# Optimization experiments

Measured on AMD Instinct MI355X. Metric: run time of the kernel, lower is better.

Reference implementation:

```python
import jax, jax.numpy as jnp
import numpy as np
from jax import lax


def _f(x, t, params):
    # Neural-ODE vector field: MLP acting on last dim (t unused, as allowed by arbitrary f)
    W1, b1, W2 = params
    return jnp.tanh(x @ W1 + b1) @ W2


def _euler_step(f, x, t, dt, params):
    return x + dt * f(x, t, params)


def _rk4_step(f, x, t, dt, params):
    # Replicates the source tableau EXACTLY, including its c-index offsets
    # (k2 uses t + c[0]*dt = t, k3 uses t + c[1]*dt, k4 uses t + c[2]*dt).
    c = (0.0, 0.5, 0.5, 1.0)
    k1 = f(x, t, params)
    k2 = f(x + dt * (0.5 * k1), t + c[0] * dt, params)
    k3 = f(x + dt * (0.5 * k2), t + c[1] * dt, params)
    k4 = f(x + dt * k3, t + c[2] * dt, params)
    return x + dt * (k1 / 6.0 + k2 / 3.0 + k3 / 3.0 + k4 / 6.0)


def _integrate(step, f, x, ts, params):
    # fixed_odeint with t = ts[k], dt = ts[k+1]-ts[k]; returns final state only
    dts = ts[1:] - ts[:-1]
    def body(xc, tdt):
        t, dt = tdt
        return step(f, xc, t, dt, params), None
    xf, _ = lax.scan(body, x, (ts[:-1], dts))
    return xf


def setup_inputs() -> dict:
    key = jax.random.key(0)
    k1, k2, k3 = jax.random.split(key, 3)
    n_sub, batch, d, h = 16, 256, 1024, 4096
    B = jax.random.normal(k1, (n_sub, batch, d), jnp.float32)
    t_span = jnp.arange(n_sub, dtype=jnp.float32)
    W1 = jax.random.normal(k2, (d, h), jnp.float32) * 0.02
    b1 = jnp.zeros((h,), jnp.float32)
    W2 = jax.random.normal(k3, (h, d), jnp.float32) * 0.02
    return {"B": B, "t_span": t_span, "W1": W1, "b1": b1, "W2": W2,
            "fine_steps": 8, "maxiter": 2}


def reference(B, t_span, W1, b1, W2, fine_steps, maxiter):
    params = (W1, b1, W2)
    n = B.shape[0]                       # n_subinterv
    dt = t_span[1] - t_span[0]
    sub_ts = jnp.linspace(0.0, dt, fine_steps)
    # Original: i = 0; while i <= maxiter: i += 1; body(i)  ->  i = 1..maxiter+1
    for i in range(1, maxiter + 2):
        # coarse (Euler) and fine (RK4) sweeps over all remaining nodes, vectorized
        B_coarse = _integrate(_euler_step, _f, B[i - 1:], sub_ts, params)  # [n-i+1,b,d]
        B_fine = _integrate(_rk4_step, _f, B[i - 1:], sub_ts, params)
        # sequential Parareal correction over nodes m = i..n-1
        def inner(B_in, cf):
            Bc, Bf = cf
            nxt = _integrate(_euler_step, _f, B_in, sub_ts, params) - Bc + Bf
            return nxt, nxt
        _, tail = lax.scan(inner, B[i - 1], (B_coarse[: n - i], B_fine[: n - i]))
        B = jnp.concatenate([B[:i], tail], axis=0)
    return B
```

## Files before the change

kernel.cpp:

```cpp
#include <hip/hip_runtime.h>
#include <cstdint>
#include <cstddef>


typedef __attribute__((ext_vector_type(4))) float f32x4;
typedef __attribute__((ext_vector_type(16))) float f32x16;
typedef __attribute__((ext_vector_type(8))) short s16x8;
typedef __attribute__((ext_vector_type(4))) unsigned short u16x4;

#define DEV __device__ __forceinline__

DEV unsigned short f2bf(float x) {
  union { float f; uint32_t u; } v; v.f = x;
  uint32_t r = v.u + 0x7FFFu + ((v.u >> 16) & 1u);
  return (unsigned short)(r >> 16);
}
DEV float bf2f(unsigned short h) {
  union { uint32_t u; float f; } v; v.u = ((uint32_t)h) << 16; return v.f;
}
DEV void split2(float x, unsigned short &h, unsigned short &l) {
  h = f2bf(x);
  l = f2bf(x - bf2f(h));
}
DEV float fast_tanh(float z) {
  return 1.f - 2.f / (__expf(2.f * z) + 1.f);
}
DEV void gload16(const unsigned short* g, unsigned short* l) {
  __builtin_amdgcn_global_load_lds(
      (const __attribute__((address_space(1))) void*)g,
      (__attribute__((address_space(3))) void*)l, 16, 0, 0);
}

DEV void swz_st(int &bx, int &by, int &bz, int STX, int STY) {
  const int gx = gridDim.x, gy = gridDim.y, gz = gridDim.z;
  const int nwg = gx * gy * gz;
  const int lin = (blockIdx.z * gy + blockIdx.y) * gx + blockIdx.x;
  const int q = nwg >> 3, r = nwg & 7;
  const int x = lin & 7, j = lin >> 3;
  const int logical = (x < r ? x * (q + 1) : r * (q + 1) + (x - r) * q) + j;
  const int plane = gx * gy;
  bz = logical / plane;
  const int p = logical % plane;
  const int bps = STX * STY;
  const int sgy = gy / STY;
  const int stid = p / bps;
  const int wid = p % bps;
  const int stx = stid / sgy;
  const int sty = stid % sgy;
  bx = stx * STX + wid % STX;
  by = sty * STY + wid / STX;
}

template<int EPI>
__global__ __launch_bounds__(256, 2) void gemm_k(
    const unsigned short* __restrict__ Ah, const unsigned short* __restrict__ Al,
    const unsigned short* __restrict__ Bh, const unsigned short* __restrict__ Bl,
    const float* __restrict__ bias,
    unsigned short* __restrict__ Oh, unsigned short* __restrict__ Ol,
    const float* __restrict__ Xin,
    float* __restrict__ ACCb,
    float* __restrict__ Xout,
    const float* __restrict__ tspan,
    float a1, float a2, int accAdd,
    int M, int N, int K, int KS, int STX, int STY)
{
  __shared__ unsigned short sA[2][128 * 64];
  __shared__ unsigned short sB[2][128 * 64];
  const int tid = threadIdx.x;
  const int w = tid >> 6, l = tid & 63;
  int bx, by, bz;
  swz_st(bx, by, bz, STX, STY);
  const int m0 = by * 128, n0 = bx * 128;
  const int wm = (w >> 1) * 64, wn = (w & 1) * 64;

  f32x16 acc[2][2];
#pragma unroll
  for (int a = 0; a < 2; ++a)
#pragma unroll
    for (int b = 0; b < 2; ++b)
#pragma unroll
      for (int r = 0; r < 16; ++r) acc[a][b][r] = 0.f;

  const int rsub = w * 8 + (l >> 3);
  const int ssrc = (l & 7) ^ (l >> 3);
  const int shalf = ssrc >> 2;
  const int schunk = ssrc & 3;
  const unsigned short* gA = (shalf ? Al : Ah) + (size_t)(m0 + rsub) * K + schunk * 8;
  const unsigned short* gB = (shalf ? Bl : Bh) + (size_t)(n0 + rsub) * K + schunk * 8;
  const size_t gstep = (size_t)32 * (size_t)K;
  const int db = w * 512;

  const int arow = l & 31;
  const int kq = l >> 5;
  const int sH[2] = { (kq) ^ (l & 7), (2 + kq) ^ (l & 7) };
  const int sL[2] = { (4 + kq) ^ (l & 7), (6 + kq) ^ (l & 7) };

  const int nk = KS >> 5;

  auto STAGE = [&](int buf, int kt) {
    const size_t ko = (size_t)kt * 32;
    unsigned short* da = &sA[buf][db];
    unsigned short* dbp = &sB[buf][db];
#pragma unroll
    for (int j = 0; j < 4; ++j) {
      gload16(gA + ko + (size_t)j * gstep, da + j * 2048);
      gload16(gB + ko + (size_t)j * gstep, dbp + j * 2048);
    }
  };

  STAGE(0, 0);
  __syncthreads();
  int cur = 0;

  for (int kt = 0; kt < nk; ++kt) {
    if (kt + 1 < nk) STAGE(cur ^ 1, kt + 1);
    const unsigned short* pa = &sA[cur][0];
    const unsigned short* pb = &sB[cur][0];
#pragma unroll
    for (int kh = 0; kh < 2; ++kh) {
      const int sh = sH[kh], sl = sL[kh];
      s16x8 bfh[2], bfl[2];
#pragma unroll
      for (int ni = 0; ni < 2; ++ni) {
        const int rb = (wn + ni * 32 + arow) * 64;
        bfh[ni] = *(const s16x8*)&pb[rb + sh * 8];
        bfl[ni] = *(const s16x8*)&pb[rb + sl * 8];
      }
#pragma unroll
      for (int mi = 0; mi < 2; ++mi) {
        const int ra = (wm + mi * 32 + arow) * 64;
        const s16x8 afh = *(const s16x8*)&pa[ra + sh * 8];
        const s16x8 afl = *(const s16x8*)&pa[ra + sl * 8];
#pragma unroll
        for (int ni = 0; ni < 2; ++ni) {
          acc[mi][ni] = __builtin_amdgcn_mfma_f32_32x32x16_bf16(afh, bfh[ni], acc[mi][ni], 0, 0, 0);
          acc[mi][ni] = __builtin_amdgcn_mfma_f32_32x32x16_bf16(afh, bfl[ni], acc[mi][ni], 0, 0, 0);
          acc[mi][ni] = __builtin_amdgcn_mfma_f32_32x32x16_bf16(afl, bfh[ni], acc[mi][ni], 0, 0, 0);
        }
      }
    }
    __syncthreads();
    cur ^= 1;
  }

  const int colb = n0 + wn + (l & 31);
  const int rowb = m0 + wm + 4 * (l >> 5);
  const float sdt = (EPI >= 3) ? (tspan[1] - tspan[0]) * (1.0f / 7.0f) : 0.f;

  if (EPI == 1) {
#pragma unroll
    for (int mi = 0; mi < 2; ++mi)
#pragma unroll
      for (int ni = 0; ni < 2; ++ni) {
        const int col = colb + ni * 32;
        const float bc = bias[col];
#pragma unroll
        for (int r = 0; r < 16; ++r) {
          const int row = rowb + mi * 32 + (r & 3) + 8 * (r >> 2);
          const size_t idx = (size_t)row * N + col;
          const float v = fast_tanh(acc[mi][ni][r] + bc);
          unsigned short hh, ll; split2(v, hh, ll);
          Oh[idx] = hh; Ol[idx] = ll;
        }
      }
  } else if (EPI == 3) {
    const float c1 = a1 * sdt, c2 = a2 * sdt;
#pragma unroll
    for (int mi = 0; mi < 2; ++mi)
#pragma unroll
      for (int ni = 0; ni < 2; ++ni) {
        const int col = colb + ni * 32;
#pragma unroll
        for (int r = 0; r < 16; ++r) {
          const int row = rowb + mi * 32 + (r & 3) + 8 * (r >> 2);
          const size_t idx = (size_t)row * N + col;
          const float f = acc[mi][ni][r];
          const float x = Xin[idx];
          const float a = (accAdd ? ACCb[idx] : x) + c1 * f;
          ACCb[idx] = a;
          const float xt = x + c2 * f;
          unsigned short hh, ll; split2(xt, hh, ll);
          Oh[idx] = hh; Ol[idx] = ll;
        }
      }
  } else {
    const float coef = a1 + a2 * sdt;
#pragma unroll
    for (int mi = 0; mi < 2; ++mi)
#pragma unroll
      for (int ni = 0; ni < 2; ++ni) {
        const int col = colb + ni * 32;
#pragma unroll
        for (int r = 0; r < 16; ++r) {
          const int row = rowb + mi * 32 + (r & 3) + 8 * (r >> 2);
          const size_t idx = (size_t)row * N + col;
          const float v = Xin[idx] + coef * acc[mi][ni][r];
          Xout[idx] = v;
          unsigned short hh, ll; split2(v, hh, ll);
          Oh[idx] = hh; Ol[idx] = ll;
        }
      }
  }
}

template<int EPI>
__global__ __launch_bounds__(256, 2) void gemm64_k(
    const unsigned short* __restrict__ Ah, const unsigned short* __restrict__ Al,
    const unsigned short* __restrict__ Bh, const unsigned short* __restrict__ Bl,
    const float* __restrict__ bias,
    float* __restrict__ Part,
    unsigned short* __restrict__ Oh, unsigned short* __restrict__ Ol,
    int M, int N, int K, int KS, int STX, int STY)
{
  __shared__ unsigned short sA[2][64 * 64];
  __shared__ unsigned short sB[2][64 * 64];
  const int tid = threadIdx.x;
  const int w = tid >> 6, l = tid & 63;
  int bx, by, bz;
  swz_st(bx, by, bz, STX, STY);
  const int m0 = by * 64, n0 = bx * 64;
  const size_t kbeg = (size_t)bz * (size_t)KS;
  const int wm = (w >> 1) * 32, wn = (w & 1) * 32;

  f32x16 acc;
#pragma unroll
  for (int r = 0; r < 16; ++r) acc[r] = 0.f;

  const int rsub = w * 8 + (l >> 3);
  const int ssrc = (l & 7) ^ (l >> 3);
  const int shalf = ssrc >> 2;
  const int schunk = ssrc & 3;
  const unsigned short* gA = (shalf ? Al : Ah) + (size_t)(m0 + rsub) * K + kbeg + schunk * 8;
  const unsigned short* gB = (shalf ? Bl : Bh) + (size_t)(n0 + rsub) * K + kbeg + schunk * 8;
  const size_t gstep = (size_t)32 * (size_t)K;
  const int db = w * 512;

  const int arow = l & 31;
  const int kq = l >> 5;
  const int sH[2] = { (kq) ^ (l & 7), (2 + kq) ^ (l & 7) };
  const int sL[2] = { (4 + kq) ^ (l & 7), (6 + kq) ^ (l & 7) };

  const int nk = KS >> 5;

  auto STAGE = [&](int buf, int kt) {
    const size_t ko = (size_t)kt * 32;
    unsigned short* da = &sA[buf][db];
    unsigned short* dbp = &sB[buf][db];
#pragma unroll
    for (int j = 0; j < 2; ++j) {
      gload16(gA + ko + (size_t)j * gstep, da + j * 2048);
      gload16(gB + ko + (size_t)j * gstep, dbp + j * 2048);
    }
  };

  STAGE(0, 0);
  __syncthreads();
  int cur = 0;

  for (int kt = 0; kt < nk; ++kt) {
    if (kt + 1 < nk) STAGE(cur ^ 1, kt + 1);
    const unsigned short* pa = &sA[cur][0];
    const unsigned short* pb = &sB[cur][0];
#pragma unroll
    for (int kh = 0; kh < 2; ++kh) {
      const int sh = sH[kh], sl = sL[kh];
      const int rb = (wn + arow) * 64;
      const int ra = (wm + arow) * 64;
      const s16x8 bfh = *(const s16x8*)&pb[rb + sh * 8];
      const s16x8 bfl = *(const s16x8*)&pb[rb + sl * 8];
      const s16x8 afh = *(const s16x8*)&pa[ra + sh * 8];
      const s16x8 afl = *(const s16x8*)&pa[ra + sl * 8];
      acc = __builtin_amdgcn_mfma_f32_32x32x16_bf16(afh, bfh, acc, 0, 0, 0);
      acc = __builtin_amdgcn_mfma_f32_32x32x16_bf16(afh, bfl, acc, 0, 0, 0);
      acc = __builtin_amdgcn_mfma_f32_32x32x16_bf16(afl, bfh, acc, 0, 0, 0);
    }
    __syncthreads();
    cur ^= 1;
  }

  const int col = n0 + wn + (l & 31);
  const int rowb = m0 + wm + 4 * (l >> 5);

  if (EPI == 1) {
    const float bc = bias[col];
#pragma unroll
    for (int r = 0; r < 16; ++r) {
      const int row = rowb + (r & 3) + 8 * (r >> 2);
      const size_t idx = (size_t)row * N + col;
      const float v = fast_tanh(acc[r] + bc);
      unsigned short hh, ll; split2(v, hh, ll);
      Oh[idx] = hh; Ol[idx] = ll;
    }
  } else {
    float* dst = Part + (size_t)bz * (size_t)M * N;
#pragma unroll
    for (int r = 0; r < 16; ++r) {
      const int row = rowb + (r & 3) + 8 * (r >> 2);
      dst[(size_t)row * N + col] = acc[r];
    }
  }
}

__global__ void reduce_axpy_k(const float* __restrict__ part, int S, int MN4,
    const float* __restrict__ tspan,
    float* __restrict__ Xf, unsigned short* __restrict__ Xh, unsigned short* __restrict__ Xl,
    const float* __restrict__ Dv, float* __restrict__ Bout, float* __restrict__ Eout)
{
  const int i = blockIdx.x * blockDim.x + threadIdx.x;
  if (i >= MN4) return;
  const float sdt = (tspan[1] - tspan[0]) * (1.0f / 7.0f);
  const size_t MN = (size_t)MN4 * 4;
  const size_t o = 4 * (size_t)i;
  f32x4 s = *(const f32x4*)(part + o);
  for (int z = 1; z < S; ++z) s += *(const f32x4*)(part + (size_t)z * MN + o);
  f32x4 e = *(const f32x4*)(Xf + o) + sdt * s;
  if (Eout) *(f32x4*)(Eout + o) = e;
  f32x4 v = e;
  if (Dv) v += *(const f32x4*)(Dv + o);
  *(f32x4*)(Xf + o) = v;
  u16x4 hh, ll;
#pragma unroll
  for (int j = 0; j < 4; ++j) { unsigned short h_, l_; split2(v[j], h_, l_); hh[j] = h_; ll[j] = l_; }
  *(u16x4*)(Xh + o) = hh;
  *(u16x4*)(Xl + o) = ll;
  if (Bout) *(f32x4*)(Bout + o) = v;
}

__global__ void axpy_split_k(
    float* __restrict__ dstF, unsigned short* __restrict__ dstH,
    unsigned short* __restrict__ dstL,
    const float* __restrict__ A, const float* __restrict__ Fv,
    float coef, int n4)
{
  for (int i = blockIdx.x * blockDim.x + threadIdx.x; i < n4;
       i += gridDim.x * blockDim.x) {
    const size_t o = 4 * (size_t)i;
    const f32x4 a = *(const f32x4*)(A + o);
    const f32x4 f = *(const f32x4*)(Fv + o);
    f32x4 v = a + coef * f;
    *(f32x4*)(dstF + o) = v;
    if (dstH) {
      u16x4 hh, ll;
#pragma unroll
      for (int j = 0; j < 4; ++j) { unsigned short h_, l_; split2(v[j], h_, l_); hh[j] = h_; ll[j] = l_; }
      *(u16x4*)(dstH + o) = hh;
      *(u16x4*)(dstL + o) = ll;
    }
  }
}

__global__ void transpose_split_k(const float* __restrict__ W,
                                  unsigned short* __restrict__ Th,
                                  unsigned short* __restrict__ Tl,
                                  int K, int N)
{
  __shared__ float t[32][33];
  const int tx = threadIdx.x & 31, ty = threadIdx.x >> 5;
  const int n0 = blockIdx.x * 32, k0 = blockIdx.y * 32;
#pragma unroll
  for (int r = 0; r < 4; ++r) {
    const int row = ty + r * 8;
    t[row][tx] = W[(size_t)(k0 + row) * N + n0 + tx];
  }
  __syncthreads();
#pragma unroll
  for (int r = 0; r < 4; ++r) {
    const int row = ty + r * 8;
    const float v = t[tx][row];
    unsigned short hh, ll; split2(v, hh, ll);
    const size_t idx = (size_t)(n0 + row) * K + k0 + tx;
    Th[idx] = hh; Tl[idx] = ll;
  }
}

extern "C" void kernel_launch(void* const* d_in, const int* in_sizes, int n_in,
                              void* d_out, int out_size, void* d_ws, size_t ws_size,
                              hipStream_t stream)
{
  const float* Bin   = (const float*)d_in[0];
  const float* tspan = (const float*)d_in[1];
  const float* W1    = (const float*)d_in[2];
  const float* b1    = (const float*)d_in[3];
  const float* W2    = (const float*)d_in[4];

  const int n = in_sizes[1];
  const int h = in_sizes[3];
  const int d = in_sizes[2] / h;
  const int batch = in_sizes[0] / (n * d);
  const int S = 7;
  const int MAXIT = 2;
  const size_t NB = (size_t)batch * d;

  float* Bw = (float*)d_out;

  uint8_t* wsb = (uint8_t*)d_ws;
  size_t off = 0;
  auto carve = [&](size_t bytes) -> void* {
    off = (off + 255) & ~(size_t)255;
    void* p = wsb + off; off += bytes; return p;
  };

  const size_t WH = (size_t)d * h;
  unsigned short* W1Th = (unsigned short*)carve(WH * 2);
  unsigned short* W1Tl = (unsigned short*)carve(WH * 2);
  unsigned short* W2Th = (unsigned short*)carve(WH * 2);
  unsigned short* W2Tl = (unsigned short*)carve(WH * 2);
  float* Dbuf = (float*)carve((size_t)(n - 1) * NB * 4);
  float* Eb   = (float*)carve((size_t)n * NB * 4);

  const int SPL2 = 4;
  float* Part = (float*)carve((size_t)SPL2 * NB * 4);

  const size_t per_node = NB * 16 + (size_t)batch * h * 4;
  int c;
  {
    size_t remb = ws_size > off + (1u << 20) ? ws_size - off - (1u << 20) : 0;
    c = (int)(remb / per_node);
    if (c < 1) c = 1;
    if (c > n - 1) c = n - 1;
  }
  const size_t CE = (size_t)c * NB;
  unsigned short* Csh = (unsigned short*)carve(CE * 2);
  unsigned short* Csl = (unsigned short*)carve(CE * 2);
  float*          Xf  = (float*)carve(CE * 4);
  unsigned short* Xh  = (unsigned short*)carve(CE * 2);
  unsigned short* Xl  = (unsigned short*)carve(CE * 2);
  float*          ACC = (float*)carve(CE * 4);
  unsigned short* Yh  = (unsigned short*)carve((size_t)c * batch * h * 2);
  unsigned short* Yl  = (unsigned short*)carve((size_t)c * batch * h * 2);
  unsigned short* XTh = Csh;
  unsigned short* XTl = Csl;

  auto pickst = [](int g, int want) {
    int s = want;
    while (s > 1 && (g % s)) s >>= 1;
    return s;
  };
  auto ewg = [](size_t n4) -> int {
    size_t g = (n4 + 255) / 256;
    if (g > 2048) g = 2048; if (g < 1) g = 1;
    return (int)g;
  };
  auto axpy = [&](float* dF, unsigned short* dH, unsigned short* dL,
                  const float* A, const float* Fv, float coef, size_t ne) {
    const int n4 = (int)(ne / 4);
    axpy_split_k<<<ewg(n4), 256, 0, stream>>>(dF, dH, dL, A, Fv, coef, n4);
  };
  auto g1 = [&](const unsigned short* xh, const unsigned short* xl, int M) {
    const int gy = M / 128;
    gemm_k<1><<<dim3(h / 128, gy, 1), 256, 0, stream>>>(
        xh, xl, W1Th, W1Tl, b1, Yh, Yl,
        nullptr, nullptr, nullptr, tspan, 0.f, 0.f, 0, M, h, d, d,
        pickst(h / 128, 8), pickst(gy, 4));
  };
  auto g2rk = [&](int M, float a1, float a2, int add) {
    const int gy = M / 128;
    gemm_k<3><<<dim3(d / 128, gy, 1), 256, 0, stream>>>(
        Yh, Yl, W2Th, W2Tl, nullptr, XTh, XTl,
        Xf, ACC, nullptr, tspan, a1, a2, add, M, d, h, h,
        pickst(d / 128, 4), pickst(gy, 4));
  };
  auto g2ax = [&](int M, float* dF, unsigned short* dH, unsigned short* dL,
                  const float* Xin, float a1, float a2) {
    const int gy = M / 128;
    gemm_k<4><<<dim3(d / 128, gy, 1), 256, 0, stream>>>(
        Yh, Yl, W2Th, W2Tl, nullptr, dH, dL,
        Xin, nullptr, dF, tspan, a1, a2, 0, M, d, h, h,
        pickst(d / 128, 4), pickst(gy, 4));
  };

  hipMemcpyAsync(Bw, Bin, (size_t)n * NB * 4, hipMemcpyDeviceToDevice, stream);
  transpose_split_k<<<dim3(h / 32, d / 32), 256, 0, stream>>>(W1, W1Th, W1Tl, d, h);
  transpose_split_k<<<dim3(d / 32, h / 32), 256, 0, stream>>>(W2, W2Th, W2Tl, h, d);

  const int MN4d = (int)(NB / 4);

  for (int i = 1; i <= MAXIT + 1; ++i) {
    const int rem = n - i;

    for (int base = 0; base < rem; base += c) {
      const int cc = (rem - base) < c ? (rem - base) : c;
      const int M = cc * batch;
      const size_t ne = (size_t)M * d;
      const int j0 = i - 1 + base;
      const float* src = Bw + (size_t)j0 * NB;
      float* Dslot = Dbuf + (size_t)base * NB;

      if (i == 1) {
        axpy(Dslot, Csh, Csl, src, src, 0.f, ne);
        for (int s = 0; s < S; ++s) {
          g1(Csh, Csl, M);
          g2ax(M, Dslot, Csh, Csl, Dslot, 0.f, 1.f);
        }
      }
      axpy(Xf, Xh, Xl, src, src, 0.f, ne);
      for (int s = 0; s < S; ++s) {
        g1(Xh, Xl, M);   g2rk(M, 1.f / 6.f, 0.5f, 0);
        g1(XTh, XTl, M); g2rk(M, 1.f / 3.f, 0.5f, 1);
        g1(XTh, XTl, M); g2rk(M, 1.f / 3.f, 1.0f, 1);
        g1(XTh, XTl, M); g2ax(M, Xf, Xh, Xl, ACC, 0.f, 1.f / 6.f);
      }
      const float* Cref = (i == 1) ? Dslot : (Eb + (size_t)j0 * NB);
      axpy(Dslot, nullptr, nullptr, Xf, Cref, -1.f, ne);
    }

    const float* start = Bw + (size_t)(i - 1) * NB;
    axpy(Xf, Xh, Xl, start, start, 0.f, NB);
    for (int m = 0; m < rem; ++m) {
      for (int s = 0; s < S; ++s) {
        gemm64_k<1><<<dim3(h / 64, batch / 64, 1), 256, 0, stream>>>(
            Xh, Xl, W1Th, W1Tl, b1, nullptr, Yh, Yl, batch, h, d, d,
            pickst(h / 64, 8), pickst(batch / 64, 4));
        gemm64_k<2><<<dim3(d / 64, batch / 64, SPL2), 256, 0, stream>>>(
            Yh, Yl, W2Th, W2Tl, nullptr, Part, nullptr, nullptr,
            batch, d, h, h / SPL2,
            pickst(d / 64, 8), pickst(batch / 64, 4));
        const bool last = (s == S - 1);
        reduce_axpy_k<<<(MN4d + 255) / 256, 256, 0, stream>>>(
            Part, SPL2, MN4d, tspan, Xf, Xh, Xl,
            last ? Dbuf + (size_t)m * NB : nullptr,
            last ? Bw + (size_t)(i + m) * NB : nullptr,
            last ? Eb + (size_t)(i - 1 + m) * NB : nullptr);
      }
    }
  }
}
```

Before: 35.28 ms.

## Add 256x256-tile 512-thread split-bf16 GEMM for large M

Adds a new GEMM kernel with 256x256 output tiles, 8 waves and double-buffered 64-wide K staging in shared memory. It is used for all three GEMM epilogues (tanh+bias, RK4 accumulate, axpy) when M is at least 2048, and the 128-tile kernel is kept for smaller M. Larger tiles raise arithmetic intensity and cut redundant global and LDS traffic per MFMA. In exchange they use 128KB of LDS, allow one block per CU, and launch fewer blocks, which can hurt latency hiding and load balance on 256 CUs.

```diff
diff --git a/kernel.cpp b/kernel.cpp
--- a/kernel.cpp
+++ b/kernel.cpp
@@ -204,6 +204,159 @@
 }
 
 template<int EPI>
+__global__ __launch_bounds__(512, 1) void gemm256_k(
+    const unsigned short* __restrict__ Ah, const unsigned short* __restrict__ Al,
+    const unsigned short* __restrict__ Bh, const unsigned short* __restrict__ Bl,
+    const float* __restrict__ bias,
+    unsigned short* __restrict__ Oh, unsigned short* __restrict__ Ol,
+    const float* __restrict__ Xin,
+    float* __restrict__ ACCb,
+    float* __restrict__ Xout,
+    const float* __restrict__ tspan,
+    float a1, float a2, int accAdd,
+    int M, int N, int K, int STX, int STY)
+{
+  __shared__ unsigned short sA[2][256 * 64];
+  __shared__ unsigned short sB[2][256 * 64];
+  const int tid = threadIdx.x;
+  const int w = tid >> 6, l = tid & 63;
+  int bx, by, bz;
+  swz_st(bx, by, bz, STX, STY);
+  const int m0 = by * 256, n0 = bx * 256;
+  const int wm = (w >> 2) * 128;
+  const int wn = (w & 3) * 64;
+
+  f32x16 acc[4][2];
+#pragma unroll
+  for (int a = 0; a < 4; ++a)
+#pragma unroll
+    for (int b = 0; b < 2; ++b)
+#pragma unroll
+      for (int r = 0; r < 16; ++r) acc[a][b][r] = 0.f;
+
+  const int rsub = w * 8 + (l >> 3);
+  const int ssrc = (l & 7) ^ (l >> 3);
+  const int shalf = ssrc >> 2;
+  const int schunk = ssrc & 3;
+  const unsigned short* gA = (shalf ? Al : Ah) + (size_t)(m0 + rsub) * K + schunk * 8;
+  const unsigned short* gB = (shalf ? Bl : Bh) + (size_t)(n0 + rsub) * K + schunk * 8;
+  const size_t gstep = (size_t)64 * (size_t)K;
+  const int db = w * 512;
+
+  const int arow = l & 31;
+  const int kq = l >> 5;
+  const int sH[2] = { (kq) ^ (l & 7), (2 + kq) ^ (l & 7) };
+  const int sL[2] = { (4 + kq) ^ (l & 7), (6 + kq) ^ (l & 7) };
+
+  const int nk = K >> 5;
+
+  auto STAGE = [&](int buf, int kt) {
+    const size_t ko = (size_t)kt * 32;
+    unsigned short* da = &sA[buf][db];
+    unsigned short* dbp = &sB[buf][db];
+#pragma unroll
+    for (int j = 0; j < 4; ++j) {
+      gload16(gA + ko + (size_t)j * gstep, da + j * 4096);
+      gload16(gB + ko + (size_t)j * gstep, dbp + j * 4096);
+    }
+  };
+
+  STAGE(0, 0);
+  __syncthreads();
+  int cur = 0;
+
+  for (int kt = 0; kt < nk; ++kt) {
+    if (kt + 1 < nk) STAGE(cur ^ 1, kt + 1);
+    const unsigned short* pa = &sA[cur][0];
+    const unsigned short* pb = &sB[cur][0];
+#pragma unroll
+    for (int kh = 0; kh < 2; ++kh) {
+      const int sh = sH[kh], sl = sL[kh];
+      s16x8 bfh[2], bfl[2];
+#pragma unroll
+      for (int ni = 0; ni < 2; ++ni) {
+        const int rb = (wn + ni * 32 + arow) * 64;
+        bfh[ni] = *(const s16x8*)&pb[rb + sh * 8];
+        bfl[ni] = *(const s16x8*)&pb[rb + sl * 8];
+      }
+#pragma unroll
+      for (int mi = 0; mi < 4; ++mi) {
+        const int ra = (wm + mi * 32 + arow) * 64;
+        const s16x8 afh = *(const s16x8*)&pa[ra + sh * 8];
+        const s16x8 afl = *(const s16x8*)&pa[ra + sl * 8];
+#pragma unroll
+        for (int ni = 0; ni < 2; ++ni) {
+          acc[mi][ni] = __builtin_amdgcn_mfma_f32_32x32x16_bf16(afh, bfh[ni], acc[mi][ni], 0, 0, 0);
+          acc[mi][ni] = __builtin_amdgcn_mfma_f32_32x32x16_bf16(afh, bfl[ni], acc[mi][ni], 0, 0, 0);
+          acc[mi][ni] = __builtin_amdgcn_mfma_f32_32x32x16_bf16(afl, bfh[ni], acc[mi][ni], 0, 0, 0);
+        }
+      }
+    }
+    __syncthreads();
+    cur ^= 1;
+  }
+
+  const int colb = n0 + wn + (l & 31);
+  const int rowb = m0 + wm + 4 * (l >> 5);
+  const float sdt = (EPI >= 3) ? (tspan[1] - tspan[0]) * (1.0f / 7.0f) : 0.f;
+
+  if (EPI == 1) {
+#pragma unroll
+    for (int mi = 0; mi < 4; ++mi)
+#pragma unroll
+      for (int ni = 0; ni < 2; ++ni) {
+        const int col = colb + ni * 32;
+        const float bc = bias[col];
+#pragma unroll
+        for (int r = 0; r < 16; ++r) {
+          const int row = rowb + mi * 32 + (r & 3) + 8 * (r >> 2);
+          const size_t idx = (size_t)row * N + col;
+          const float v = fast_tanh(acc[mi][ni][r] + bc);
+          unsigned short hh, ll; split2(v, hh, ll);
+          Oh[idx] = hh; Ol[idx] = ll;
+        }
+      }
+  } else if (EPI == 3) {
+    const float c1 = a1 * sdt, c2 = a2 * sdt;
+#pragma unroll
+    for (int mi = 0; mi < 4; ++mi)
+#pragma unroll
+      for (int ni = 0; ni < 2; ++ni) {
+        const int col = colb + ni * 32;
+#pragma unroll
+        for (int r = 0; r < 16; ++r) {
+          const int row = rowb + mi * 32 + (r & 3) + 8 * (r >> 2);
+          const size_t idx = (size_t)row * N + col;
+          const float f = acc[mi][ni][r];
+          const float x = Xin[idx];
+          const float a = (accAdd ? ACCb[idx] : x) + c1 * f;
+          ACCb[idx] = a;
+          const float xt = x + c2 * f;
+          unsigned short hh, ll; split2(xt, hh, ll);
+          Oh[idx] = hh; Ol[idx] = ll;
+        }
+      }
+  } else {
+    const float coef = a1 + a2 * sdt;
+#pragma unroll
+    for (int mi = 0; mi < 4; ++mi)
+#pragma unroll
+      for (int ni = 0; ni < 2; ++ni) {
+        const int col = colb + ni * 32;
+#pragma unroll
+        for (int r = 0; r < 16; ++r) {
+          const int row = rowb + mi * 32 + (r & 3) + 8 * (r >> 2);
+          const size_t idx = (size_t)row * N + col;
+          const float v = Xin[idx] + coef * acc[mi][ni][r];
+          Xout[idx] = v;
+          unsigned short hh, ll; split2(v, hh, ll);
+          Oh[idx] = hh; Ol[idx] = ll;
+        }
+      }
+  }
+}
+
+template<int EPI>
 __global__ __launch_bounds__(256, 2) void gemm64_k(
     const unsigned short* __restrict__ Ah, const unsigned short* __restrict__ Al,
     const unsigned short* __restrict__ Bh, const unsigned short* __restrict__ Bl,
@@ -446,27 +599,52 @@
     const int n4 = (int)(ne / 4);
     axpy_split_k<<<ewg(n4), 256, 0, stream>>>(dF, dH, dL, A, Fv, coef, n4);
   };
+
   auto g1 = [&](const unsigned short* xh, const unsigned short* xl, int M) {
-    const int gy = M / 128;
-    gemm_k<1><<<dim3(h / 128, gy, 1), 256, 0, stream>>>(
-        xh, xl, W1Th, W1Tl, b1, Yh, Yl,
-        nullptr, nullptr, nullptr, tspan, 0.f, 0.f, 0, M, h, d, d,
-        pickst(h / 128, 8), pickst(gy, 4));
+    if (M >= 2048) {
+      const int gy = M / 256;
+      gemm256_k<1><<<dim3(h / 256, gy, 1), 512, 0, stream>>>(
+          xh, xl, W1Th, W1Tl, b1, Yh, Yl,
+          nullptr, nullptr, nullptr, tspan, 0.f, 0.f, 0, M, h, d,
+          pickst(h / 256, 2), pickst(gy, 2));
+    } else {
+      const int gy = M / 128;
+      gemm_k<1><<<dim3(h / 128, gy, 1), 256, 0, stream>>>(
+          xh, xl, W1Th, W1Tl, b1, Yh, Yl,
+          nullptr, nullptr, nullptr, tspan, 0.f, 0.f, 0, M, h, d, d,
+          pickst(h / 128, 8), pickst(gy, 4));
+    }
   };
   auto g2rk = [&](int M, float a1, float a2, int add) {
-    const int gy = M / 128;
-    gemm_k<3><<<dim3(d / 128, gy, 1), 256, 0, stream>>>(
-        Yh, Yl, W2Th, W2Tl, nullptr, XTh, XTl,
-        Xf, ACC, nullptr, tspan, a1, a2, add, M, d, h, h,
-        pickst(d / 128, 4), pickst(gy, 4));
+    if (M >= 2048) {
+      const int gy = M / 256;
+      gemm256_k<3><<<dim3(d / 256, gy, 1), 512, 0, stream>>>(
+          Yh, Yl, W2Th, W2Tl, nullptr, XTh, XTl,
+          Xf, ACC, nullptr, tspan, a1, a2, add, M, d, h,
+          pickst(d / 256, 2), pickst(gy, 2));
+    } else {
+      const int gy = M / 128;
+      gemm_k<3><<<dim3(d / 128, gy, 1), 256, 0, stream>>>(
+          Yh, Yl, W2Th, W2Tl, nullptr, XTh, XTl,
+          Xf, ACC, nullptr, tspan, a1, a2, add, M, d, h, h,
+          pickst(d / 128, 4), pickst(gy, 4));
+    }
   };
   auto g2ax = [&](int M, float* dF, unsigned short* dH, unsigned short* dL,
                   const float* Xin, float a1, float a2) {
-    const int gy = M / 128;
-    gemm_k<4><<<dim3(d / 128, gy, 1), 256, 0, stream>>>(
-        Yh, Yl, W2Th, W2Tl, nullptr, dH, dL,
-        Xin, nullptr, dF, tspan, a1, a2, 0, M, d, h, h,
-        pickst(d / 128, 4), pickst(gy, 4));
+    if (M >= 2048) {
+      const int gy = M / 256;
+      gemm256_k<4><<<dim3(d / 256, gy, 1), 512, 0, stream>>>(
+          Yh, Yl, W2Th, W2Tl, nullptr, dH, dL,
+          Xin, nullptr, dF, tspan, a1, a2, 0, M, d, h,
+          pickst(d / 256, 2), pickst(gy, 2));
+    } else {
+      const int gy = M / 128;
+      gemm_k<4><<<dim3(d / 128, gy, 1), 256, 0, stream>>>(
+          Yh, Yl, W2Th, W2Tl, nullptr, dH, dL,
+          Xin, nullptr, dF, tspan, a1, a2, 0, M, d, h, h,
+          pickst(d / 128, 4), pickst(gy, 4));
+    }
   };
 
   hipMemcpyAsync(Bw, Bin, (size_t)n * NB * 4, hipMemcpyDeviceToDevice, stream);
```

Result: slower. 46.89 ms (+32.9%).
